# Kernel optimization log

Measured on AMD Instinct MI355X. Metric: run time of the kernel, lower is better.

The kernel has to match this reference:

```python
import jax, jax.numpy as jnp
import numpy as np

EMBED_DIM = 1024
NUM_HEADS = 16
HEAD_DIM = EMBED_DIM // NUM_HEADS
LN_EPS = 1e-5


def setup_inputs() -> dict:
    key = jax.random.key(0)
    ks = jax.random.split(key, 5)
    N, L, C = 32, 577, EMBED_DIM
    x = jax.random.normal(ks[0], (N, L, C), dtype=jnp.float32)
    ln1_g = jnp.ones((C,), dtype=jnp.float32)
    ln1_b = jnp.zeros((C,), dtype=jnp.float32)
    w_in = jax.random.normal(ks[1], (3 * C, C), dtype=jnp.float32) * (C ** -0.5)
    b_in = jax.random.normal(ks[2], (3 * C,), dtype=jnp.float32) * 0.02
    w_out = jax.random.normal(ks[3], (C, C), dtype=jnp.float32) * (C ** -0.5)
    b_out = jax.random.normal(ks[4], (C,), dtype=jnp.float32) * 0.02
    return {"x": x, "ln1_g": ln1_g, "ln1_b": ln1_b, "w_in": w_in,
            "b_in": b_in, "w_out": w_out, "b_out": b_out}


def _layernorm(x, g, b):
    mu = jnp.mean(x, axis=-1, keepdims=True)
    var = jnp.mean(jnp.square(x - mu), axis=-1, keepdims=True)
    return (x - mu) * jax.lax.rsqrt(var + LN_EPS) * g + b


def reference(x, ln1_g, ln1_b, w_in, b_in, w_out, b_out):
    # ClearCLIP last block, attn_variant='qq', keep_residual=False, keep_ffn=False.
    N, L, C = x.shape
    H, D = NUM_HEADS, HEAD_DIM
    z = _layernorm(x, ln1_g, ln1_b)
    qkv = z @ w_in.T + b_in                      # (N, L, 3C)
    q, k, v = jnp.split(qkv, 3, axis=-1)
    k = q                                        # 'qq' self-self variant
    def heads(t):
        return t.reshape(N, L, H, D).transpose(0, 2, 1, 3)  # (N, H, L, D)
    q, k, v = heads(q), heads(k), heads(v)
    scale = 1.0 / np.sqrt(D).astype(np.float32)
    scores = jnp.einsum('nhld,nhsd->nhls', q, k) * scale    # (N, H, L, L)
    attn = jax.nn.softmax(scores, axis=-1)
    out = jnp.einsum('nhls,nhsd->nhld', attn, v)            # (N, H, L, D)
    out = out.transpose(0, 2, 1, 3).reshape(N, L, C)
    return out @ w_out.T + b_out                 # ls_1 = Identity, no residual/FFN
```

## Files before the change

kernel.cpp:

```cpp
#include <hip/hip_runtime.h>
#include <stdint.h>

typedef short bf16x8 __attribute__((ext_vector_type(8)));
typedef float f32x4 __attribute__((ext_vector_type(4)));
typedef unsigned int uint4v __attribute__((ext_vector_type(4)));
typedef unsigned short ushort4v __attribute__((ext_vector_type(4)));
typedef float float4v __attribute__((ext_vector_type(4)));

#define MROWS 18464
#define SEQ   577
#define CDIM  1024
#define SPAD  640
#define W1ELEMS (2048*1024)
#define W2ELEMS (1024*1024)
#define SQC 0.42466089f

__device__ __forceinline__ unsigned short f2bf(float f) {
  unsigned int u = __float_as_uint(f);
  u += 0x7fffu + ((u >> 16) & 1u);
  return (unsigned short)(u >> 16);
}

__device__ __forceinline__ void load_lds16(const void* g, void* lds) {
  __builtin_amdgcn_global_load_lds(
      (const __attribute__((address_space(1))) unsigned int*)(uint64_t)(uintptr_t)g,
      (__attribute__((address_space(3))) unsigned int*)(unsigned int)(uintptr_t)lds,
      16, 0, 0);
}

__global__ __launch_bounds__(256) void ln_kernel(const float* __restrict__ x,
                                                 const float* __restrict__ g,
                                                 const float* __restrict__ b,
                                                 unsigned short* __restrict__ z) {
  const int row = blockIdx.x;
  const int t = threadIdx.x;
  const float4v v = *(const float4v*)(x + (size_t)row * CDIM + t * 4);
  float s  = v[0] + v[1] + v[2] + v[3];
  float ss = v[0]*v[0] + v[1]*v[1] + v[2]*v[2] + v[3]*v[3];
  #pragma unroll
  for (int off = 1; off < 64; off <<= 1) { s += __shfl_xor(s, off); ss += __shfl_xor(ss, off); }
  __shared__ float rs[4], rss[4];
  const int w = t >> 6, l = t & 63;
  if (l == 0) { rs[w] = s; rss[w] = ss; }
  __syncthreads();
  s = rs[0] + rs[1] + rs[2] + rs[3];
  ss = rss[0] + rss[1] + rss[2] + rss[3];
  const float mu = s * (1.0f / CDIM);
  const float var = ss * (1.0f / CDIM) - mu * mu;
  const float rstd = rsqrtf(var + 1e-5f);
  const float4v gv = *(const float4v*)(g + t * 4);
  const float4v bv = *(const float4v*)(b + t * 4);
  ushort4v o;
  #pragma unroll
  for (int j = 0; j < 4; ++j) o[j] = f2bf((v[j] - mu) * rstd * gv[j] + bv[j]);
  *(ushort4v*)(z + (size_t)row * CDIM + t * 4) = o;
}

__global__ __launch_bounds__(256) void conv_kernel(const float* __restrict__ w_in,
                                                   const float* __restrict__ w_out,
                                                   unsigned short* __restrict__ wqv,
                                                   unsigned short* __restrict__ wo,
                                                   unsigned short* __restrict__ vt) {
  const int idx = blockIdx.x * 256 + threadIdx.x;
  const int e = idx * 4;
  if (e < W1ELEMS) {
    const int row = e >> 10;
    const int srow = row < 1024 ? row : row + 1024;
    const float4v v = *(const float4v*)(w_in + (size_t)srow * 1024 + (e & 1023));
    ushort4v o;
    #pragma unroll
    for (int j = 0; j < 4; ++j) o[j] = f2bf(v[j]);
    *(ushort4v*)(wqv + e) = o;
  } else if (e < W1ELEMS + W2ELEMS) {
    const int e2 = e - W1ELEMS;
    const float4v v = *(const float4v*)(w_out + e2);
    ushort4v o;
    #pragma unroll
    for (int j = 0; j < 4; ++j) o[j] = f2bf(v[j]);
    *(ushort4v*)(wo + e2) = o;
  } else {
    const int pidx = idx - (W1ELEMS + W2ELEMS) / 4;
    const int ic = pidx >> 3, part = pidx & 7;
    *(uint4v*)(vt + (size_t)ic * SPAD + 576 + part * 8) = (uint4v)0u;
  }
}

template<int MODE>
__global__ __launch_bounds__(1024, 4) void gemm256(const unsigned short* __restrict__ A,
                                                   const unsigned short* __restrict__ B,
                                                   const float* __restrict__ bias,
                                                   void* __restrict__ outp,
                                                   unsigned short* __restrict__ vtout) {
  __shared__ char smem[131072];
  const int t = threadIdx.x;
  const int w = t >> 6, l = t & 63;
  int p, c;
  if constexpr (MODE == 0) {
    const int L = (blockIdx.x & 7) * 73 + (blockIdx.x >> 3);
    p = L >> 3; c = L & 7;
  } else {
    const int xcd = blockIdx.x & 7, j = blockIdx.x >> 3;
    const int L = (xcd < 4 ? xcd * 37 : 148 + (xcd - 4) * 36) + j;
    p = L >> 2; c = L & 3;
  }
  const int m0 = p * 256, n0 = c * 256;
  const int wm = w >> 2, wn = w & 3;
  const int g4 = (l >> 4) * 4;
  const int fr = l & 15;
  const int fb = (l >> 4) * 16;
  const int sw = (l & 7) << 4;

  f32x4 acc[4][4];
  #pragma unroll
  for (int i = 0; i < 4; ++i)
    #pragma unroll
    for (int j = 0; j < 4; ++j) acc[i][j] = (f32x4)0.0f;

  const int srow = l >> 3;
  const int scol = ((((l & 7) * 16) ^ ((srow & 7) << 4)) >> 1);
  int ra0 = m0 + w * 16 + srow;     if (ra0 > MROWS - 1) ra0 = MROWS - 1;
  int ra1 = m0 + w * 16 + 8 + srow; if (ra1 > MROWS - 1) ra1 = MROWS - 1;
  const unsigned short* pA0 = A + (size_t)ra0 * 1024 + scol;
  const unsigned short* pA1 = A + (size_t)ra1 * 1024 + scol;
  const unsigned short* pB0 = B + (size_t)(n0 + w * 16 + srow) * 1024 + scol;
  const unsigned short* pB1 = pB0 + (size_t)8 * 1024;

  #define STG(kt, buf)                                                     \
    {                                                                      \
      char* const dA_ = smem + (buf) * 65536 + w * 2048;                   \
      char* const dB_ = dA_ + 32768;                                       \
      const int k0_ = (kt) * 64;                                           \
      load_lds16(pA0 + k0_, dA_);                                          \
      load_lds16(pA1 + k0_, dA_ + 1024);                                   \
      load_lds16(pB0 + k0_, dB_);                                          \
      load_lds16(pB1 + k0_, dB_ + 1024);                                   \
    }

  STG(0, 0)
  __syncthreads();

  for (int kb = 0; kb < 16; ++kb) {
    const int b = kb & 1;
    if (kb < 15) STG(kb + 1, b ^ 1)
    const char* Ab = smem + b * 65536;
    const char* Bb = Ab + 32768;
    #pragma unroll
    for (int kk = 0; kk < 2; ++kk) {
      bf16x8 af[4], bfr[4];
      #pragma unroll
      for (int i = 0; i < 4; ++i)
        af[i] = *(const bf16x8*)(Ab + (wm * 64 + i * 16 + fr) * 128 + ((kk * 64 + fb) ^ sw));
      #pragma unroll
      for (int j = 0; j < 4; ++j)
        bfr[j] = *(const bf16x8*)(Bb + (wn * 64 + j * 16 + fr) * 128 + ((kk * 64 + fb) ^ sw));
      #pragma unroll
      for (int i = 0; i < 4; ++i)
        #pragma unroll
        for (int j = 0; j < 4; ++j)
          acc[i][j] = __builtin_amdgcn_mfma_f32_16x16x32_bf16(af[i], bfr[j], acc[i][j], 0, 0, 0);
    }
    __syncthreads();
  }
  #undef STG

  if constexpr (MODE == 0) {
    unsigned short* sm = (unsigned short*)smem;
    const bool isq = (n0 < 1024);
    const float* bb = isq ? (bias + n0) : (bias + 1024 + n0);
    const float scl = isq ? SQC : 1.0f;
    float bcol[4];
    #pragma unroll
    for (int j = 0; j < 4; ++j) bcol[j] = bb[wn * 64 + j * 16 + fr];
    for (int pass = 0; pass < 4; ++pass) {
      if (wm == pass) {
        #pragma unroll
        for (int i = 0; i < 4; ++i)
          #pragma unroll
          for (int j = 0; j < 4; ++j)
            #pragma unroll
            for (int r = 0; r < 4; ++r)
              sm[(i * 16 + g4 + r) * 264 + wn * 64 + j * 16 + fr] =
                  f2bf((acc[i][j][r] + bcol[j]) * scl);
      }
      __syncthreads();
      if (isq) {
        unsigned short* o = (unsigned short*)outp;
        #pragma unroll
        for (int it = 0; it < 2; ++it) {
          const int cid = it * 1024 + t;
          const int row = cid >> 5, ch = cid & 31;
          const int grow = m0 + pass * 64 + row;
          if (grow < MROWS)
            *(uint4v*)(o + (size_t)grow * 1024 + n0 + ch * 8) =
                *(const uint4v*)(sm + row * 264 + ch * 8);
        }
      } else {
        const int tokloc = t & 63, chgrp = t >> 6;
        const int token = m0 + pass * 64 + tokloc;
        if (token < MROWS) {
          const unsigned int nimg = (unsigned int)token / 577u;
          const int s = token - (int)(nimg * 577u);
          unsigned short* op =
              vtout + ((size_t)nimg * 1024 + (n0 - 1024) + chgrp * 16) * SPAD + s;
          const unsigned short* sp = sm + tokloc * 264 + chgrp * 16;
          #pragma unroll 8
          for (int it = 0; it < 16; ++it)
            op[(size_t)it * SPAD] = sp[it];
        }
      }
      __syncthreads();
    }
  } else {
    float* smf = (float*)smem;
    float bcol[4];
    #pragma unroll
    for (int j = 0; j < 4; ++j) bcol[j] = bias[n0 + wn * 64 + j * 16 + fr];
    float* o = (float*)outp;
    for (int pass = 0; pass < 4; ++pass) {
      if (wm == pass) {
        #pragma unroll
        for (int i = 0; i < 4; ++i)
          #pragma unroll
          for (int j = 0; j < 4; ++j)
            #pragma unroll
            for (int r = 0; r < 4; ++r)
              smf[(i * 16 + g4 + r) * 260 + wn * 64 + j * 16 + fr] =
                  acc[i][j][r] + bcol[j];
      }
      __syncthreads();
      #pragma unroll
      for (int it = 0; it < 4; ++it) {
        const int cid = it * 1024 + t;
        const int row = cid >> 6, ch = cid & 63;
        const int grow = m0 + pass * 64 + row;
        if (grow < MROWS)
          *(float4v*)(o + (size_t)grow * 1024 + n0 + ch * 4) =
              *(const float4v*)(smf + row * 260 + ch * 4);
      }
      __syncthreads();
    }
  }
}

__global__ __launch_bounds__(256) void attn_kernel(const unsigned short* __restrict__ qbuf,
                                                   const unsigned short* __restrict__ vt,
                                                   unsigned short* __restrict__ out) {
  __shared__ char smem[32768];
  const int t = threadIdx.x, w = t >> 6, l = t & 63;
  const int g = l >> 4, fr = l & 15;
  const int bid = blockIdx.x;
  const int xcd = bid & 7, idx = bid >> 3;
  const int nhl = idx / 5;
  const int qb = idx - nhl * 5;
  const int nh = xcd * 64 + nhl;
  const int n = nh >> 4, h = nh & 15;
  const size_t rowbase = (size_t)n * SEQ;
  const int sw = (l & 7) << 4;

  bf16x8 bq[2][2];
  #pragma unroll
  for (int half = 0; half < 2; ++half) {
    const unsigned short* qp =
        qbuf + (rowbase + qb * 128 + half * 64 + w * 16 + fr) * 1024 + h * 64 + g * 8;
    bq[half][0] = *(const bf16x8*)qp;
    bq[half][1] = *(const bf16x8*)(qp + 32);
  }

  const int srow = l >> 3;
  const int scolE = ((((l & 7) * 16) ^ ((srow & 7) << 4)) >> 1);
  const unsigned short* ksrc = qbuf + (rowbase + w * 16 + srow) * 1024 + h * 64 + scolE;
  const unsigned short* vsrc = vt + ((size_t)nh * 64 + w * 16 + srow) * SPAD + scolE;

  f32x4 acc[2][4];
  #pragma unroll
  for (int half = 0; half < 2; ++half)
    #pragma unroll
    for (int cf = 0; cf < 4; ++cf) acc[half][cf] = (f32x4)0.0f;
  float l_run[2] = {0.0f, 0.0f};

  {
    char* kdst = smem + (w * 16) * 128;
    char* vdst = smem + 8192 + (w * 16) * 128;
    load_lds16(ksrc, kdst);
    load_lds16(ksrc + (size_t)8 * 1024, kdst + 1024);
    load_lds16(vsrc, vdst);
    load_lds16(vsrc + 8 * SPAD, vdst + 1024);
  }
  __syncthreads();

  for (int kb = 0; kb < 10; ++kb) {
    const int b = kb & 1;
    const char* kbuf = smem + b * 16384;
    const char* vbuf = kbuf + 8192;

    if (kb < 9) {
      char* kdst = smem + (b ^ 1) * 16384 + (w * 16) * 128;
      char* vdst = kdst + 8192;
      load_lds16(ksrc + (size_t)((kb + 1) * 64) * 1024, kdst);
      load_lds16(ksrc + (size_t)((kb + 1) * 64 + 8) * 1024, kdst + 1024);
      load_lds16(vsrc + (kb + 1) * 64, vdst);
      load_lds16(vsrc + 8 * SPAD + (kb + 1) * 64, vdst + 1024);
    }

    f32x4 s4[2][4];
    #pragma unroll
    for (int half = 0; half < 2; ++half)
      #pragma unroll
      for (int cf = 0; cf < 4; ++cf) s4[half][cf] = (f32x4)0.0f;
    #pragma unroll
    for (int kk = 0; kk < 2; ++kk)
      #pragma unroll
      for (int cf = 0; cf < 4; ++cf) {
        const bf16x8 af = *(const bf16x8*)(kbuf + (cf * 16 + fr) * 128 + ((kk * 64 + g * 16) ^ sw));
        s4[0][cf] = __builtin_amdgcn_mfma_f32_16x16x32_bf16(af, bq[0][kk], s4[0][cf], 0, 0, 0);
        s4[1][cf] = __builtin_amdgcn_mfma_f32_16x16x32_bf16(af, bq[1][kk], s4[1][cf], 0, 0, 0);
      }

    if (kb == 9) {
      #pragma unroll
      for (int half = 0; half < 2; ++half) {
        #pragma unroll
        for (int cf = 0; cf < 4; ++cf)
          #pragma unroll
          for (int r = 0; r < 4; ++r)
            if (cf != 0 || r != 0) s4[half][cf][r] = -__builtin_inff();
        s4[half][0][0] = (g == 0) ? s4[half][0][0] : -__builtin_inff();
      }
    }

    bf16x8 ap[2][2];
    #pragma unroll
    for (int half = 0; half < 2; ++half) {
      float sum = 0.0f;
      #pragma unroll
      for (int cf = 0; cf < 4; ++cf)
        #pragma unroll
        for (int r = 0; r < 4; ++r) {
          const float p2 = __builtin_amdgcn_exp2f(s4[half][cf][r]);
          s4[half][cf][r] = p2;
          sum += p2;
        }
      sum += __shfl_xor(sum, 16);
      sum += __shfl_xor(sum, 32);
      l_run[half] += sum;

      unsigned int pka[4], pkb[4];
      #pragma unroll
      for (int cf = 0; cf < 4; ++cf) {
        asm("v_cvt_pk_bf16_f32 %0, %1, %2" : "=v"(pka[cf]) : "v"(s4[half][cf][0]), "v"(s4[half][cf][1]));
        asm("v_cvt_pk_bf16_f32 %0, %1, %2" : "=v"(pkb[cf]) : "v"(s4[half][cf][2]), "v"(s4[half][cf][3]));
      }
      #pragma unroll
      for (int kk = 0; kk < 2; ++kk) {
        unsigned int a0 = pka[2 * kk], b0 = pka[2 * kk + 1];
        unsigned int a1 = pkb[2 * kk], b1 = pkb[2 * kk + 1];
        asm("v_permlane32_swap_b32 %0, %1" : "+v"(a0), "+v"(b0));
        asm("v_permlane16_swap_b32 %0, %1" : "+v"(a0), "+v"(b0));
        asm("v_permlane32_swap_b32 %0, %1" : "+v"(a1), "+v"(b1));
        asm("v_permlane16_swap_b32 %0, %1" : "+v"(a1), "+v"(b1));
        union { unsigned int i[4]; bf16x8 v; } u;
        u.i[0] = a0; u.i[1] = a1; u.i[2] = b0; u.i[3] = b1;
        ap[half][kk] = u.v;
      }
    }

    #pragma unroll
    for (int kk = 0; kk < 2; ++kk)
      #pragma unroll
      for (int cf = 0; cf < 4; ++cf) {
        const bf16x8 bv = *(const bf16x8*)(vbuf + (cf * 16 + fr) * 128 + ((kk * 64 + g * 16) ^ sw));
        acc[0][cf] = __builtin_amdgcn_mfma_f32_16x16x32_bf16(ap[0][kk], bv, acc[0][cf], 0, 0, 0);
        acc[1][cf] = __builtin_amdgcn_mfma_f32_16x16x32_bf16(ap[1][kk], bv, acc[1][cf], 0, 0, 0);
      }

    __syncthreads();
  }

  #pragma unroll
  for (int half = 0; half < 2; ++half) {
    const float rcp = 1.0f / l_run[half];
    #pragma unroll
    for (int r = 0; r < 4; ++r) {
      const float rr = __shfl(rcp, g * 4 + r);
      const int qg = qb * 128 + half * 64 + w * 16 + g * 4 + r;
      if (qg < SEQ) {
        #pragma unroll
        for (int cf = 0; cf < 4; ++cf)
          out[(rowbase + qg) * 1024 + h * 64 + cf * 16 + fr] = f2bf(acc[half][cf][r] * rr);
      }
    }
  }
}

extern "C" void kernel_launch(void* const* d_in, const int* in_sizes, int n_in,
                              void* d_out, int out_size, void* d_ws, size_t ws_size,
                              hipStream_t stream) {
  const float* x     = (const float*)d_in[0];
  const float* ln_g  = (const float*)d_in[1];
  const float* ln_b  = (const float*)d_in[2];
  const float* w_in  = (const float*)d_in[3];
  const float* b_in  = (const float*)d_in[4];
  const float* w_out = (const float*)d_in[5];
  const float* b_out = (const float*)d_in[6];

  unsigned short* z    = (unsigned short*)d_ws;
  unsigned short* qbuf = z + (size_t)MROWS * 1024;
  unsigned short* vt   = qbuf + (size_t)MROWS * 1024;
  unsigned short* wqv  = vt + (size_t)512 * 64 * SPAD;
  unsigned short* wo   = wqv + (size_t)2048 * 1024;

  ln_kernel<<<MROWS, 256, 0, stream>>>(x, ln_g, ln_b, z);
  conv_kernel<<<4096, 256, 0, stream>>>(w_in, w_out, wqv, wo, vt);
  gemm256<0><<<584, 1024, 0, stream>>>(z, wqv, b_in, qbuf, vt);
  attn_kernel<<<2560, 256, 0, stream>>>(qbuf, vt, z);
  gemm256<1><<<292, 1024, 0, stream>>>(z, wo, b_out, d_out, nullptr);
}
```

Measured before the change: 248.0 us.

## Split GEMMs into QV and proj kernels with 4-slot K32 async pipeline

Replaces the templated double-buffered GEMM (K-tile 64) with a 4-slot ring of K-tile 32 stages. Loads run two stages ahead, each iteration waits with a manual vmcnt and a single s_barrier instead of a trailing __syncthreads, and s_setprio raises priority around the MFMA block. The output-projection GEMM becomes its own kernel with 512 threads, each wave holding an 8x4 accumulator tile. The goal is to overlap global-to-LDS loads with MFMA work and cut barrier stalls, at the cost of higher register pressure in the proj kernel and fragile hand-written waitcnt logic.

```diff
diff --git a/kernel.cpp b/kernel.cpp
--- a/kernel.cpp
+++ b/kernel.cpp
@@ -85,30 +85,28 @@
   }
 }
 
-template<int MODE>
-__global__ __launch_bounds__(1024, 4) void gemm256(const unsigned short* __restrict__ A,
+#define VMC2 { asm volatile("s_waitcnt vmcnt(2)" ::: "memory"); }
+#define VMC4 { asm volatile("s_waitcnt vmcnt(4)" ::: "memory"); }
+#define VMC0 { asm volatile("s_waitcnt vmcnt(0)" ::: "memory"); }
+#define SB0  __builtin_amdgcn_sched_barrier(0);
+#define BARR __builtin_amdgcn_s_barrier();
+
+__global__ __launch_bounds__(1024, 4) void gemm_qv(const unsigned short* __restrict__ A,
                                                    const unsigned short* __restrict__ B,
                                                    const float* __restrict__ bias,
-                                                   void* __restrict__ outp,
+                                                   unsigned short* __restrict__ qout,
                                                    unsigned short* __restrict__ vtout) {
   __shared__ char smem[131072];
   const int t = threadIdx.x;
   const int w = t >> 6, l = t & 63;
-  int p, c;
-  if constexpr (MODE == 0) {
-    const int L = (blockIdx.x & 7) * 73 + (blockIdx.x >> 3);
-    p = L >> 3; c = L & 7;
-  } else {
-    const int xcd = blockIdx.x & 7, j = blockIdx.x >> 3;
-    const int L = (xcd < 4 ? xcd * 37 : 148 + (xcd - 4) * 36) + j;
-    p = L >> 2; c = L & 3;
-  }
+  const int L = (blockIdx.x & 7) * 73 + (blockIdx.x >> 3);
+  const int p = L >> 3, c = L & 7;
   const int m0 = p * 256, n0 = c * 256;
   const int wm = w >> 2, wn = w & 3;
   const int g4 = (l >> 4) * 4;
   const int fr = l & 15;
-  const int fb = (l >> 4) * 16;
-  const int sw = (l & 7) << 4;
+  const int g = l >> 4;
+  const int rswz = ((fr >> 1) & 3) << 4;
 
   f32x4 acc[4][4];
   #pragma unroll
@@ -116,129 +114,186 @@
     #pragma unroll
     for (int j = 0; j < 4; ++j) acc[i][j] = (f32x4)0.0f;
 
-  const int srow = l >> 3;
-  const int scol = ((((l & 7) * 16) ^ ((srow & 7) << 4)) >> 1);
-  int ra0 = m0 + w * 16 + srow;     if (ra0 > MROWS - 1) ra0 = MROWS - 1;
-  int ra1 = m0 + w * 16 + 8 + srow; if (ra1 > MROWS - 1) ra1 = MROWS - 1;
-  const unsigned short* pA0 = A + (size_t)ra0 * 1024 + scol;
-  const unsigned short* pA1 = A + (size_t)ra1 * 1024 + scol;
-  const unsigned short* pB0 = B + (size_t)(n0 + w * 16 + srow) * 1024 + scol;
-  const unsigned short* pB1 = pB0 + (size_t)8 * 1024;
-
-  #define STG(kt, buf)                                                     \
-    {                                                                      \
-      char* const dA_ = smem + (buf) * 65536 + w * 2048;                   \
-      char* const dB_ = dA_ + 32768;                                       \
-      const int k0_ = (kt) * 64;                                           \
-      load_lds16(pA0 + k0_, dA_);                                          \
-      load_lds16(pA1 + k0_, dA_ + 1024);                                   \
-      load_lds16(pB0 + k0_, dB_);                                          \
-      load_lds16(pB1 + k0_, dB_ + 1024);                                   \
-    }
-
-  STG(0, 0)
+  const int dchunk = ((l & 3) ^ ((l >> 3) & 3)) * 8;
+  int ra = m0 + w * 16 + (l >> 2); if (ra > MROWS - 1) ra = MROWS - 1;
+  const unsigned short* pA = A + (size_t)ra * 1024 + dchunk;
+  const unsigned short* pB = B + (size_t)(n0 + w * 16 + (l >> 2)) * 1024 + dchunk;
+  const int ldst = w * 1024 + l * 16;
+
+  #define QSTG(kt, slot)                                   \
+    {                                                      \
+      char* const d_ = smem + (slot) * 32768 + ldst;       \
+      load_lds16(pA + (kt) * 32, d_);                      \
+      load_lds16(pB + (kt) * 32, d_ + 16384);              \
+    }
+
+  QSTG(0, 0) QSTG(1, 1)
+
+  for (int kb = 0; kb < 32; ++kb) {
+    if (kb < 31) VMC2 else VMC0
+    SB0 BARR SB0
+    const char* Ab = smem + (kb & 3) * 32768;
+    const char* Bb = Ab + 16384;
+    bf16x8 af[4], bf[4];
+    #pragma unroll
+    for (int i = 0; i < 4; ++i)
+      af[i] = *(const bf16x8*)(Ab + (wm * 64 + i * 16 + fr) * 64 + ((g * 16) ^ rswz));
+    #pragma unroll
+    for (int j = 0; j < 4; ++j)
+      bf[j] = *(const bf16x8*)(Bb + (wn * 64 + j * 16 + fr) * 64 + ((g * 16) ^ rswz));
+    __builtin_amdgcn_s_setprio(1);
+    #pragma unroll
+    for (int i = 0; i < 4; ++i)
+      #pragma unroll
+      for (int j = 0; j < 4; ++j)
+        acc[i][j] = __builtin_amdgcn_mfma_f32_16x16x32_bf16(af[i], bf[j], acc[i][j], 0, 0, 0);
+    __builtin_amdgcn_s_setprio(0);
+    if (kb < 30) QSTG(kb + 2, (kb + 2) & 3)
+  }
+  #undef QSTG
   __syncthreads();
 
-  for (int kb = 0; kb < 16; ++kb) {
-    const int b = kb & 1;
-    if (kb < 15) STG(kb + 1, b ^ 1)
-    const char* Ab = smem + b * 65536;
-    const char* Bb = Ab + 32768;
-    #pragma unroll
-    for (int kk = 0; kk < 2; ++kk) {
-      bf16x8 af[4], bfr[4];
-      #pragma unroll
-      for (int i = 0; i < 4; ++i)
-        af[i] = *(const bf16x8*)(Ab + (wm * 64 + i * 16 + fr) * 128 + ((kk * 64 + fb) ^ sw));
-      #pragma unroll
-      for (int j = 0; j < 4; ++j)
-        bfr[j] = *(const bf16x8*)(Bb + (wn * 64 + j * 16 + fr) * 128 + ((kk * 64 + fb) ^ sw));
+  unsigned short* sm = (unsigned short*)smem;
+  const bool isq = (n0 < 1024);
+  const float* bb = isq ? (bias + n0) : (bias + 1024 + n0);
+  const float scl = isq ? SQC : 1.0f;
+  float bcol[4];
+  #pragma unroll
+  for (int j = 0; j < 4; ++j) bcol[j] = bb[wn * 64 + j * 16 + fr];
+  for (int pass = 0; pass < 4; ++pass) {
+    if (wm == pass) {
       #pragma unroll
       for (int i = 0; i < 4; ++i)
         #pragma unroll
         for (int j = 0; j < 4; ++j)
-          acc[i][j] = __builtin_amdgcn_mfma_f32_16x16x32_bf16(af[i], bfr[j], acc[i][j], 0, 0, 0);
+          #pragma unroll
+          for (int r = 0; r < 4; ++r)
+            sm[(i * 16 + g4 + r) * 264 + wn * 64 + j * 16 + fr] =
+                f2bf((acc[i][j][r] + bcol[j]) * scl);
     }
     __syncthreads();
-  }
-  #undef STG
-
-  if constexpr (MODE == 0) {
-    unsigned short* sm = (unsigned short*)smem;
-    const bool isq = (n0 < 1024);
-    const float* bb = isq ? (bias + n0) : (bias + 1024 + n0);
-    const float scl = isq ? SQC : 1.0f;
-    float bcol[4];
-    #pragma unroll
-    for (int j = 0; j < 4; ++j) bcol[j] = bb[wn * 64 + j * 16 + fr];
-    for (int pass = 0; pass < 4; ++pass) {
-      if (wm == pass) {
-        #pragma unroll
-        for (int i = 0; i < 4; ++i)
-          #pragma unroll
-          for (int j = 0; j < 4; ++j)
-            #pragma unroll
-            for (int r = 0; r < 4; ++r)
-              sm[(i * 16 + g4 + r) * 264 + wn * 64 + j * 16 + fr] =
-                  f2bf((acc[i][j][r] + bcol[j]) * scl);
-      }
-      __syncthreads();
-      if (isq) {
-        unsigned short* o = (unsigned short*)outp;
-        #pragma unroll
-        for (int it = 0; it < 2; ++it) {
-          const int cid = it * 1024 + t;
-          const int row = cid >> 5, ch = cid & 31;
-          const int grow = m0 + pass * 64 + row;
-          if (grow < MROWS)
-            *(uint4v*)(o + (size_t)grow * 1024 + n0 + ch * 8) =
-                *(const uint4v*)(sm + row * 264 + ch * 8);
-        }
-      } else {
-        const int tokloc = t & 63, chgrp = t >> 6;
-        const int token = m0 + pass * 64 + tokloc;
-        if (token < MROWS) {
-          const unsigned int nimg = (unsigned int)token / 577u;
-          const int s = token - (int)(nimg * 577u);
-          unsigned short* op =
-              vtout + ((size_t)nimg * 1024 + (n0 - 1024) + chgrp * 16) * SPAD + s;
-          const unsigned short* sp = sm + tokloc * 264 + chgrp * 16;
-          #pragma unroll 8
-          for (int it = 0; it < 16; ++it)
-            op[(size_t)it * SPAD] = sp[it];
-        }
-      }
-      __syncthreads();
-    }
-  } else {
-    float* smf = (float*)smem;
-    float bcol[4];
-    #pragma unroll
-    for (int j = 0; j < 4; ++j) bcol[j] = bias[n0 + wn * 64 + j * 16 + fr];
-    float* o = (float*)outp;
-    for (int pass = 0; pass < 4; ++pass) {
-      if (wm == pass) {
-        #pragma unroll
-        for (int i = 0; i < 4; ++i)
-          #pragma unroll
-          for (int j = 0; j < 4; ++j)
-            #pragma unroll
-            for (int r = 0; r < 4; ++r)
-              smf[(i * 16 + g4 + r) * 260 + wn * 64 + j * 16 + fr] =
-                  acc[i][j][r] + bcol[j];
-      }
-      __syncthreads();
-      #pragma unroll
-      for (int it = 0; it < 4; ++it) {
+    if (isq) {
+      #pragma unroll
+      for (int it = 0; it < 2; ++it) {
         const int cid = it * 1024 + t;
-        const int row = cid >> 6, ch = cid & 63;
+        const int row = cid >> 5, ch = cid & 31;
         const int grow = m0 + pass * 64 + row;
         if (grow < MROWS)
-          *(float4v*)(o + (size_t)grow * 1024 + n0 + ch * 4) =
-              *(const float4v*)(smf + row * 260 + ch * 4);
-      }
-      __syncthreads();
-    }
+          *(uint4v*)(qout + (size_t)grow * 1024 + n0 + ch * 8) =
+              *(const uint4v*)(sm + row * 264 + ch * 8);
+      }
+    } else {
+      const int tokloc = t & 63, chgrp = t >> 6;
+      const int token = m0 + pass * 64 + tokloc;
+      if (token < MROWS) {
+        const unsigned int nimg = (unsigned int)token / 577u;
+        const int s = token - (int)(nimg * 577u);
+        unsigned short* op =
+            vtout + ((size_t)nimg * 1024 + (n0 - 1024) + chgrp * 16) * SPAD + s;
+        const unsigned short* sp = sm + tokloc * 264 + chgrp * 16;
+        #pragma unroll 8
+        for (int it = 0; it < 16; ++it)
+          op[(size_t)it * SPAD] = sp[it];
+      }
+    }
+    __syncthreads();
+  }
+}
+
+__global__ __launch_bounds__(512, 2) void gemm_proj(const unsigned short* __restrict__ A,
+                                                    const unsigned short* __restrict__ B,
+                                                    const float* __restrict__ bias,
+                                                    float* __restrict__ outp) {
+  __shared__ char smem[131072];
+  const int t = threadIdx.x;
+  const int w = t >> 6, l = t & 63;
+  const int xcd = blockIdx.x & 7, j0 = blockIdx.x >> 3;
+  const int L = (xcd < 4 ? xcd * 37 : 148 + (xcd - 4) * 36) + j0;
+  const int p = L >> 2, c = L & 3;
+  const int m0 = p * 256, n0 = c * 256;
+  const int wm = w >> 2, wn = w & 3;
+  const int g4 = (l >> 4) * 4;
+  const int fr = l & 15;
+  const int g = l >> 4;
+  const int rswz = ((fr >> 1) & 3) << 4;
+
+  f32x4 acc[8][4];
+  #pragma unroll
+  for (int i = 0; i < 8; ++i)
+    #pragma unroll
+    for (int j = 0; j < 4; ++j) acc[i][j] = (f32x4)0.0f;
+
+  const int dchunk = ((l & 3) ^ ((l >> 3) & 3)) * 8;
+  int ra0 = m0 + w * 32 + (l >> 2);      if (ra0 > MROWS - 1) ra0 = MROWS - 1;
+  int ra1 = m0 + w * 32 + 16 + (l >> 2); if (ra1 > MROWS - 1) ra1 = MROWS - 1;
+  const unsigned short* pA0 = A + (size_t)ra0 * 1024 + dchunk;
+  const unsigned short* pA1 = A + (size_t)ra1 * 1024 + dchunk;
+  const unsigned short* pB0 = B + (size_t)(n0 + w * 32 + (l >> 2)) * 1024 + dchunk;
+  const unsigned short* pB1 = pB0 + (size_t)16 * 1024;
+  const int ldst = w * 2048 + l * 16;
+
+  #define PSTG(kt, slot)                                   \
+    {                                                      \
+      char* const d_ = smem + (slot) * 32768 + ldst;       \
+      load_lds16(pA0 + (kt) * 32, d_);                     \
+      load_lds16(pA1 + (kt) * 32, d_ + 1024);              \
+      load_lds16(pB0 + (kt) * 32, d_ + 16384);             \
+      load_lds16(pB1 + (kt) * 32, d_ + 17408);             \
+    }
+
+  PSTG(0, 0) PSTG(1, 1)
+
+  for (int kb = 0; kb < 32; ++kb) {
+    if (kb < 31) VMC4 else VMC0
+    SB0 BARR SB0
+    const char* Ab = smem + (kb & 3) * 32768;
+    const char* Bb = Ab + 16384;
+    bf16x8 af[8], bf[4];
+    #pragma unroll
+    for (int i = 0; i < 8; ++i)
+      af[i] = *(const bf16x8*)(Ab + (wm * 128 + i * 16 + fr) * 64 + ((g * 16) ^ rswz));
+    #pragma unroll
+    for (int j = 0; j < 4; ++j)
+      bf[j] = *(const bf16x8*)(Bb + (wn * 64 + j * 16 + fr) * 64 + ((g * 16) ^ rswz));
+    __builtin_amdgcn_s_setprio(1);
+    #pragma unroll
+    for (int i = 0; i < 8; ++i)
+      #pragma unroll
+      for (int j = 0; j < 4; ++j)
+        acc[i][j] = __builtin_amdgcn_mfma_f32_16x16x32_bf16(af[i], bf[j], acc[i][j], 0, 0, 0);
+    __builtin_amdgcn_s_setprio(0);
+    if (kb < 30) PSTG(kb + 2, (kb + 2) & 3)
+  }
+  #undef PSTG
+  __syncthreads();
+
+  float* smf = (float*)smem;
+  float bcol[4];
+  #pragma unroll
+  for (int j = 0; j < 4; ++j) bcol[j] = bias[n0 + wn * 64 + j * 16 + fr];
+  for (int q4 = 0; q4 < 4; ++q4) {
+    if (wm == (q4 >> 1)) {
+      const int i0 = (q4 & 1) * 4;
+      #pragma unroll
+      for (int i2 = 0; i2 < 4; ++i2)
+        #pragma unroll
+        for (int j = 0; j < 4; ++j)
+          #pragma unroll
+          for (int r = 0; r < 4; ++r)
+            smf[(i2 * 16 + g4 + r) * 260 + wn * 64 + j * 16 + fr] =
+                acc[i0 + i2][j][r] + bcol[j];
+    }
+    __syncthreads();
+    #pragma unroll
+    for (int it = 0; it < 8; ++it) {
+      const int cid = it * 512 + t;
+      const int row = cid >> 6, ch = cid & 63;
+      const int grow = m0 + q4 * 64 + row;
+      if (grow < MROWS)
+        *(float4v*)(outp + (size_t)grow * 1024 + n0 + ch * 4) =
+            *(const float4v*)(smf + row * 260 + ch * 4);
+    }
+    __syncthreads();
   }
 }
 
@@ -411,7 +466,7 @@
 
   ln_kernel<<<MROWS, 256, 0, stream>>>(x, ln_g, ln_b, z);
   conv_kernel<<<4096, 256, 0, stream>>>(w_in, w_out, wqv, wo, vt);
-  gemm256<0><<<584, 1024, 0, stream>>>(z, wqv, b_in, qbuf, vt);
+  gemm_qv<<<584, 1024, 0, stream>>>(z, wqv, b_in, qbuf, vt);
   attn_kernel<<<2560, 256, 0, stream>>>(qbuf, vt, z);
-  gemm256<1><<<292, 1024, 0, stream>>>(z, wo, b_out, d_out, nullptr);
-}
+  gemm_proj<<<292, 512, 0, stream>>>(z, wo, b_out, (float*)d_out);
+}
```

New measurement: 261.7 us. 5.5% more time.
